# Kernel tuning notes

Measured on AMD Instinct MI355X. Metric: run time of the kernel, lower is better.

## Reference

```python
import jax, jax.numpy as jnp
import numpy as np

RES = 128
SH_DIM = 9            # (deg+1)^2, deg=2
CH = SH_DIM * 3 + 1   # 28: 3*9 SH rgb coeffs + 1 sigma
AABB_MIN = -1.0
AABB_MAX = 1.0
STEP = (AABB_MAX - AABB_MIN) / (RES - 1)   # voxel_len = mean(aabb_size/(res-1))
UNIFORM = 0.5
N_SAMPLES = int(RES * 3 / UNIFORM)         # plenoxels count: 768
EPS = 1e-10


def sh_encode_deg2(d):
    # real spherical harmonics basis, degree 2 (9 coefficients), on normalized dirs
    d = d / jnp.linalg.norm(d, axis=-1, keepdims=True)
    x, y, z = d[..., 0], d[..., 1], d[..., 2]
    C0 = 0.28209479177387814
    C1 = 0.4886025119029199
    C20, C21, C22 = 1.0925484305920792, -1.0925484305920792, 0.31539156525252005
    C23, C24 = -1.0925484305920792, 0.5462742152960396
    return jnp.stack([
        jnp.full_like(x, C0),
        -C1 * y, C1 * z, -C1 * x,
        C20 * x * y, C21 * y * z, C22 * (2.0 * z * z - x * x - y * y),
        C23 * x * z, C24 * (x * x - y * y),
    ], axis=-1)


def grid_sample_3d(grid, pts):
    # grid: [D,H,W,C]; pts: [...,3] in [-1,1], (x,y,z) with x->W, y->H, z->D.
    # Matches torch F.grid_sample(mode='bilinear', padding_mode='zeros', align_corners=True).
    D, H, W, C = grid.shape
    lead = pts.shape[:-1]
    p = pts.reshape(-1, 3)
    x = (p[:, 0] + 1.0) * 0.5 * (W - 1)
    y = (p[:, 1] + 1.0) * 0.5 * (H - 1)
    z = (p[:, 2] + 1.0) * 0.5 * (D - 1)
    x0f, y0f, z0f = jnp.floor(x), jnp.floor(y), jnp.floor(z)
    fx, fy, fz = x - x0f, y - y0f, z - z0f
    x0 = x0f.astype(jnp.int32)
    y0 = y0f.astype(jnp.int32)
    z0 = z0f.astype(jnp.int32)
    flat = grid.reshape(-1, C)
    out = jnp.zeros((p.shape[0], C), grid.dtype)
    for dz in (0, 1):
        for dy in (0, 1):
            for dx in (0, 1):
                xi, yi, zi = x0 + dx, y0 + dy, z0 + dz
                valid = (xi >= 0) & (xi < W) & (yi >= 0) & (yi < H) & (zi >= 0) & (zi < D)
                w = ((fx if dx else 1.0 - fx)
                     * (fy if dy else 1.0 - fy)
                     * (fz if dz else 1.0 - fz)) * valid
                idx = (jnp.clip(zi, 0, D - 1) * H + jnp.clip(yi, 0, H - 1)) * W + jnp.clip(xi, 0, W - 1)
                out = out + w[:, None] * flat[idx]
    return out.reshape(lead + (C,))


def setup_inputs() -> dict:
    key = jax.random.key(0)
    k1, k2, k3 = jax.random.split(key, 3)
    B = 4096
    # origins on a radius-3 sphere, aimed at jittered targets inside the unit box
    o = jax.random.normal(k1, (B, 3), dtype=jnp.float32)
    rays_o = 3.0 * o / jnp.linalg.norm(o, axis=-1, keepdims=True)
    tgt = jax.random.uniform(k2, (B, 3), dtype=jnp.float32, minval=-0.5, maxval=0.5)
    d = tgt - rays_o
    rays_d = d / jnp.linalg.norm(d, axis=-1, keepdims=True)
    grid_data = 0.1 * jax.random.normal(k3, (RES ** 3, CH), dtype=jnp.float32)
    grid_data = grid_data.at[:, -1].add(0.1)  # ini_sigma offset
    return {"rays_d": rays_d, "rays_o": rays_o, "grid_data": grid_data}


def reference(rays_d, rays_o, grid_data):
    B = rays_d.shape[0]
    aabb_lo = jnp.full((3,), AABB_MIN, rays_o.dtype)
    aabb_hi = jnp.full((3,), AABB_MAX, rays_o.dtype)
    # ray-AABB intersection (no_grad in torch)
    t_pos = (aabb_hi - rays_o) / rays_d
    t_neg = (aabb_lo - rays_o) / rays_d
    t_in = jnp.minimum(t_pos, t_neg)
    t_out = jnp.maximum(t_pos, t_neg)
    start = jnp.max(t_in, axis=-1)                  # [B]
    stop = jnp.min(t_out, axis=-1, keepdims=True)   # [B,1]
    # tensor_linspace from start+u*step to start+u*step*n, then clamp max=stop
    w = jnp.linspace(0.0, 1.0, N_SAMPLES, dtype=rays_o.dtype)  # [S]
    s0 = start + UNIFORM * STEP
    s1 = start + UNIFORM * STEP * N_SAMPLES
    intersections = s0[:, None] * (1.0 - w) + s1[:, None] * w   # [B,S]
    intersections = jnp.minimum(intersections, stop)
    t = intersections[:, :-1]                                    # [B,S-1]
    pts = rays_o[:, None, :] + t[:, :, None] * rays_d[:, None, :]
    pts = (pts - AABB_MIN) * (2.0 / (AABB_MAX - AABB_MIN)) - 1.0  # normalize to [-1,1]
    # trilinear sample of the voxel grid (torch layout: D=res0,H=res1,W=res2; x->W)
    interp = grid_sample_3d(grid_data.reshape(RES, RES, RES, CH), pts)  # [B,S-1,CH]
    sigma = interp[..., -1]
    rgb_sh = interp[..., :-1].reshape(B, N_SAMPLES - 1, 3, SH_DIM)
    sh = sh_encode_deg2(rays_d)                                   # [B,9]
    rgb = jnp.einsum('bsck,bk->bsc', rgb_sh, sh)
    # volumetric rendering
    dists = jnp.diff(intersections, axis=1) * jnp.linalg.norm(rays_d, axis=-1, keepdims=True)
    alpha = 1.0 - jnp.exp(-jax.nn.relu(sigma) * dists)
    cum_light = jnp.concatenate(
        [jnp.ones((B, 1), alpha.dtype), jnp.cumprod(1.0 - alpha[:, :-1] + EPS, axis=-1)], axis=-1)
    abs_light = alpha * cum_light
    acc_map = abs_light.sum(-1)
    rgb_map = (abs_light[..., None] * jax.nn.sigmoid(rgb)).sum(-2)
    depth = (abs_light * t).sum(-1)
    rgb_map = rgb_map + (1.0 - acc_map[:, None])  # white background
    return rgb_map, alpha, depth
```

## Files before the change

### kernel.cpp

```cpp
#include <hip/hip_runtime.h>
#include <math.h>

#define RESG 128
#define CHG 28
#define NT 767
#define NBKT 384

__global__ __launch_bounds__(1024) void prep_sort(
    const float* __restrict__ rays_d, int* __restrict__ perm, int B)
{
    __shared__ int cnt[NBKT];
    __shared__ int off[NBKT];
    __shared__ unsigned short keys[4096];
    const int tid = threadIdx.x;
    for (int i = tid; i < NBKT; i += 1024) cnt[i] = 0;
    __syncthreads();
    for (int r = tid; r < B; r += 1024) {
        float ddx = rays_d[r*3+0], ddy = rays_d[r*3+1], ddz = rays_d[r*3+2];
        float ax = fabsf(ddx), ay = fabsf(ddy), az = fabsf(ddz);
        int face; float u, v, m;
        if (ax >= ay && ax >= az) { face = (ddx < 0.f) ? 0 : 1; m = ax; u = ddy; v = ddz; }
        else if (ay >= az)        { face = (ddy < 0.f) ? 2 : 3; m = ay; u = ddx; v = ddz; }
        else                      { face = (ddz < 0.f) ? 4 : 5; m = az; u = ddx; v = ddy; }
        float iu = u / m * 0.5f + 0.5f;
        float iv = v / m * 0.5f + 0.5f;
        int qu = min(7, max(0, (int)(iu * 8.0f)));
        int qv = min(7, max(0, (int)(iv * 8.0f)));
        int k = face * 64 + qu * 8 + qv;
        keys[r] = (unsigned short)k;
        atomicAdd(&cnt[k], 1);
    }
    __syncthreads();
    if (tid == 0) {
        int a = 0;
        for (int i = 0; i < NBKT; ++i) { off[i] = a; a += cnt[i]; }
    }
    __syncthreads();
    for (int r = tid; r < B; r += 1024) {
        int k = keys[r];
        int slot = atomicAdd(&off[k], 1);
        perm[slot] = r;
    }
}

__global__ __launch_bounds__(256) void nerf_grid_kernel(
    const float* __restrict__ rays_d,
    const float* __restrict__ rays_o,
    const float* __restrict__ grid,
    const int*   __restrict__ perm,
    float* __restrict__ out_rgb,
    float* __restrict__ out_alpha,
    float* __restrict__ out_depth)
{
    const int ray  = perm[blockIdx.x];
    const int tid  = threadIdx.x;
    const int lane = tid & 63;
    const int wave = tid >> 6;

    const float EPSC   = 1e-10f;
    const float INV127 = 1.0f / 127.0f;

    __shared__ float a_lds[NT + 1];
    __shared__ float r_lds[NT + 1];
    __shared__ float g_lds[NT + 1];
    __shared__ float b_lds[NT + 1];
    __shared__ float wprod[4];
    __shared__ float red[4][5];

    const float ox = rays_o[ray*3+0], oy = rays_o[ray*3+1], oz = rays_o[ray*3+2];
    const float dx = rays_d[ray*3+0], dy = rays_d[ray*3+1], dz = rays_d[ray*3+2];
    const float dnorm = sqrtf(dx*dx + dy*dy + dz*dz);

    float txp = (1.0f - ox)/dx, txn = (-1.0f - ox)/dx;
    float typ = (1.0f - oy)/dy, tyn = (-1.0f - oy)/dy;
    float tzp = (1.0f - oz)/dz, tzn = (-1.0f - oz)/dz;
    const float start = fmaxf(fmaxf(fminf(txp,txn), fminf(typ,tyn)), fminf(tzp,tzn));
    const float stop  = fminf(fminf(fmaxf(txp,txn), fmaxf(typ,tyn)), fmaxf(tzp,tzn));

    int n_proc = (int)((stop - start) * 127.0f) + 2;
    n_proc = n_proc < 0 ? 0 : (n_proc > NT ? NT : n_proc);

    const float inv = 1.0f/dnorm;
    const float nx = dx*inv, ny = dy*inv, nz = dz*inv;
    float sh0, sh1, sh2, sh3, sh4, sh5, sh6, sh7, sh8;
    {
        const float C0 = 0.28209479177387814f;
        const float C1 = 0.4886025119029199f;
        const float C20 = 1.0925484305920792f, C21 = -1.0925484305920792f;
        const float C22 = 0.31539156525252005f;
        const float C23 = -1.0925484305920792f, C24 = 0.5462742152960396f;
        sh0 = C0;   sh1 = -C1*ny; sh2 = C1*nz; sh3 = -C1*nx;
        sh4 = C20*nx*ny; sh5 = C21*ny*nz;
        sh6 = C22*(2.0f*nz*nz - nx*nx - ny*ny);
        sh7 = C23*nx*nz; sh8 = C24*(nx*nx - ny*ny);
    }

    const int samp   = lane >> 3;
    const int corner = lane & 7;
    const int cdx = corner & 1, cdy = (corner >> 1) & 1, cdz = corner >> 2;

    for (int base = wave*8; base < n_proc; base += 32) {
        const int s = base + samp;
        float rr = 0.0f, gg = 0.0f, bb = 0.0f, sg = 0.0f;
        float t0 = 0.0f, dist = 0.0f;
        bool live = false;
        if (s < n_proc) {
            t0 = fminf(start + (float)(s+1)*INV127, stop);
            const float t1 = fminf(start + (float)(s+2)*INV127, stop);
            dist = (t1 - t0) * dnorm;
            live = dist > 0.0f;
        }
        if (live) {
            const float gx = (ox + t0*dx + 1.0f)*63.5f;
            const float gy = (oy + t0*dy + 1.0f)*63.5f;
            const float gz = (oz + t0*dz + 1.0f)*63.5f;
            const float fx0 = floorf(gx), fy0 = floorf(gy), fz0 = floorf(gz);
            const float fx = gx - fx0, fy = gy - fy0, fz = gz - fz0;
            const int xi = (int)fx0 + cdx;
            const int yi = (int)fy0 + cdy;
            const int zi = (int)fz0 + cdz;
            const bool valid = ((unsigned)xi < (unsigned)RESG) &
                               ((unsigned)yi < (unsigned)RESG) &
                               ((unsigned)zi < (unsigned)RESG);
            const float w = (cdx ? fx : 1.0f-fx) *
                            (cdy ? fy : 1.0f-fy) *
                            (cdz ? fz : 1.0f-fz);
            if (valid && w != 0.0f) {
                const float4* row = (const float4*)(grid + (size_t)(((zi*RESG) + yi)*RESG + xi)*CHG);
                const float4 v0 = row[0], v1 = row[1], v2 = row[2], v3 = row[3];
                const float4 v4 = row[4], v5 = row[5], v6 = row[6];
                rr = w*(v0.x*sh0 + v0.y*sh1 + v0.z*sh2 + v0.w*sh3 +
                        v1.x*sh4 + v1.y*sh5 + v1.z*sh6 + v1.w*sh7 + v2.x*sh8);
                gg = w*(v2.y*sh0 + v2.z*sh1 + v2.w*sh2 + v3.x*sh3 +
                        v3.y*sh4 + v3.z*sh5 + v3.w*sh6 + v4.x*sh7 + v4.y*sh8);
                bb = w*(v4.z*sh0 + v4.w*sh1 + v5.x*sh2 + v5.y*sh3 +
                        v5.z*sh4 + v5.w*sh5 + v6.x*sh6 + v6.y*sh7 + v6.z*sh8);
                sg = w*v6.w;
            }
        }
        #pragma unroll
        for (int off2 = 1; off2 < 8; off2 <<= 1) {
            rr += __shfl_xor(rr, off2, 64);
            gg += __shfl_xor(gg, off2, 64);
            bb += __shfl_xor(bb, off2, 64);
            sg += __shfl_xor(sg, off2, 64);
        }
        if (corner == 0 && s < n_proc) {
            a_lds[s] = live ? 1.0f - expf(-fmaxf(sg, 0.0f)*dist) : 0.0f;
            r_lds[s] = 1.0f/(1.0f + expf(-rr));
            g_lds[s] = 1.0f/(1.0f + expf(-gg));
            b_lds[s] = 1.0f/(1.0f + expf(-bb));
        }
    }
    __syncthreads();

    for (int s = tid; s < NT; s += 256)
        out_alpha[(size_t)ray*NT + s] = (s < n_proc) ? a_lds[s] : 0.0f;

    float a_r[3], q_r[3], t_r[3], rr_r[3], gg_r[3], bb_r[3];
    #pragma unroll
    for (int k = 0; k < 3; ++k) {
        const int s = tid*3 + k;
        float a = 0.0f, rr = 0.0f, gg = 0.0f, bb = 0.0f, tt = 0.0f;
        if (s < NT) {
            tt = fminf(start + (float)(s+1)*INV127, stop);
            if (s < n_proc) {
                a = a_lds[s];
                rr = r_lds[s]; gg = g_lds[s]; bb = b_lds[s];
            }
        }
        a_r[k] = a; q_r[k] = (s < NT) ? (1.0f - a + EPSC) : 1.0f;
        t_r[k] = tt; rr_r[k] = rr; gg_r[k] = gg; bb_r[k] = bb;
    }

    const float P = q_r[0]*q_r[1]*q_r[2];
    float incl = P;
    #pragma unroll
    for (int off2 = 1; off2 < 64; off2 <<= 1) {
        const float n = __shfl_up(incl, off2, 64);
        if (lane >= off2) incl *= n;
    }
    float excl = __shfl_up(incl, 1, 64);
    if (lane == 0) excl = 1.0f;

    if (lane == 63) wprod[wave] = incl;
    __syncthreads();
    float wpre = 1.0f;
    for (int w2 = 0; w2 < 4; ++w2) if (w2 < wave) wpre *= wprod[w2];

    float cum = wpre * excl;
    float accA = 0.0f, accR = 0.0f, accG = 0.0f, accB = 0.0f, accD = 0.0f;
    #pragma unroll
    for (int k = 0; k < 3; ++k) {
        const float abs_l = a_r[k] * cum;
        accA += abs_l;
        accR += abs_l * rr_r[k];
        accG += abs_l * gg_r[k];
        accB += abs_l * bb_r[k];
        accD += abs_l * t_r[k];
        cum *= q_r[k];
    }

    #pragma unroll
    for (int off2 = 32; off2 > 0; off2 >>= 1) {
        accA += __shfl_down(accA, off2, 64);
        accR += __shfl_down(accR, off2, 64);
        accG += __shfl_down(accG, off2, 64);
        accB += __shfl_down(accB, off2, 64);
        accD += __shfl_down(accD, off2, 64);
    }
    if (lane == 0) {
        red[wave][0] = accA; red[wave][1] = accR; red[wave][2] = accG;
        red[wave][3] = accB; red[wave][4] = accD;
    }
    __syncthreads();
    if (tid == 0) {
        float A = 0.0f, R = 0.0f, G = 0.0f, Bv = 0.0f, D = 0.0f;
        #pragma unroll
        for (int w2 = 0; w2 < 4; ++w2) {
            A += red[w2][0]; R += red[w2][1]; G += red[w2][2];
            Bv += red[w2][3]; D += red[w2][4];
        }
        const float bg = 1.0f - A;
        out_rgb[ray*3+0] = R  + bg;
        out_rgb[ray*3+1] = G  + bg;
        out_rgb[ray*3+2] = Bv + bg;
        out_depth[ray] = D;
    }
}

extern "C" void kernel_launch(void* const* d_in, const int* in_sizes, int n_in,
                              void* d_out, int out_size, void* d_ws, size_t ws_size,
                              hipStream_t stream) {
    const float* rays_d = (const float*)d_in[0];
    const float* rays_o = (const float*)d_in[1];
    const float* grid   = (const float*)d_in[2];
    const int B = in_sizes[0] / 3;

    float* out       = (float*)d_out;
    float* out_rgb   = out;
    float* out_alpha = out + (size_t)B*3;
    float* out_depth = out + (size_t)B*3 + (size_t)B*NT;

    int* perm = (int*)d_ws;

    prep_sort<<<1, 1024, 0, stream>>>(rays_d, perm, B);
    nerf_grid_kernel<<<B, 256, 0, stream>>>(rays_d, rays_o, grid, perm,
                                            out_rgb, out_alpha, out_depth);
}
```

Measured before the change: 89.35 us.

## Sort rays by sample count for load balance and use ds_swizzle reductions

The ray-ordering pass now buckets rays by their AABB intersection length (the number of live samples) in descending order, instead of by direction cube-face cells. Long rays are then dispatched first, so the GPU finishes with short blocks and tail imbalance shrinks, at the cost of direction coherence between neighbouring blocks. The bucket prefix sum now uses a wave scan instead of a serial loop. The 8-lane butterfly reductions in the main kernel are replaced with ds_swizzle XOR patterns, which avoid the more general cross-lane permute path.

```diff
diff --git a/kernel.cpp b/kernel.cpp
--- a/kernel.cpp
+++ b/kernel.cpp
@@ -4,41 +4,52 @@
 #define RESG 128
 #define CHG 28
 #define NT 767
-#define NBKT 384
+#define NLBKT 48
+
+template <int PAT>
+static __device__ __forceinline__ float swz(float x) {
+    return __int_as_float(__builtin_amdgcn_ds_swizzle(__float_as_int(x), PAT));
+}
 
 __global__ __launch_bounds__(1024) void prep_sort(
-    const float* __restrict__ rays_d, int* __restrict__ perm, int B)
+    const float* __restrict__ rays_d, const float* __restrict__ rays_o,
+    int* __restrict__ perm, int B)
 {
-    __shared__ int cnt[NBKT];
-    __shared__ int off[NBKT];
-    __shared__ unsigned short keys[4096];
+    __shared__ int cnt[64];
+    __shared__ int off[64];
+    __shared__ unsigned char keys[4096];
     const int tid = threadIdx.x;
-    for (int i = tid; i < NBKT; i += 1024) cnt[i] = 0;
+    if (tid < 64) cnt[tid] = 0;
     __syncthreads();
     for (int r = tid; r < B; r += 1024) {
-        float ddx = rays_d[r*3+0], ddy = rays_d[r*3+1], ddz = rays_d[r*3+2];
-        float ax = fabsf(ddx), ay = fabsf(ddy), az = fabsf(ddz);
-        int face; float u, v, m;
-        if (ax >= ay && ax >= az) { face = (ddx < 0.f) ? 0 : 1; m = ax; u = ddy; v = ddz; }
-        else if (ay >= az)        { face = (ddy < 0.f) ? 2 : 3; m = ay; u = ddx; v = ddz; }
-        else                      { face = (ddz < 0.f) ? 4 : 5; m = az; u = ddx; v = ddy; }
-        float iu = u / m * 0.5f + 0.5f;
-        float iv = v / m * 0.5f + 0.5f;
-        int qu = min(7, max(0, (int)(iu * 8.0f)));
-        int qv = min(7, max(0, (int)(iv * 8.0f)));
-        int k = face * 64 + qu * 8 + qv;
-        keys[r] = (unsigned short)k;
+        const float ox = rays_o[r*3+0], oy = rays_o[r*3+1], oz = rays_o[r*3+2];
+        const float dx = rays_d[r*3+0], dy = rays_d[r*3+1], dz = rays_d[r*3+2];
+        float txp = (1.0f - ox)/dx, txn = (-1.0f - ox)/dx;
+        float typ = (1.0f - oy)/dy, tyn = (-1.0f - oy)/dy;
+        float tzp = (1.0f - oz)/dz, tzn = (-1.0f - oz)/dz;
+        const float start = fmaxf(fmaxf(fminf(txp,txn), fminf(typ,tyn)), fminf(tzp,tzn));
+        const float stop  = fminf(fminf(fmaxf(txp,txn), fmaxf(typ,tyn)), fmaxf(tzp,tzn));
+        int n_proc = (int)((stop - start) * 127.0f) + 2;
+        n_proc = n_proc < 0 ? 0 : (n_proc > NT ? NT : n_proc);
+        int lvl = n_proc >> 4; if (lvl > NLBKT-1) lvl = NLBKT-1;
+        const int k = (NLBKT-1) - lvl;
+        keys[r] = (unsigned char)k;
         atomicAdd(&cnt[k], 1);
     }
     __syncthreads();
-    if (tid == 0) {
-        int a = 0;
-        for (int i = 0; i < NBKT; ++i) { off[i] = a; a += cnt[i]; }
+    if (tid < 64) {
+        int v = cnt[tid];
+        int incl = v;
+        #pragma unroll
+        for (int o2 = 1; o2 < 64; o2 <<= 1) {
+            const int n = __shfl_up(incl, o2, 64);
+            if ((tid & 63) >= o2) incl += n;
+        }
+        off[tid] = incl - v;
     }
     __syncthreads();
     for (int r = tid; r < B; r += 1024) {
-        int k = keys[r];
-        int slot = atomicAdd(&off[k], 1);
+        const int slot = atomicAdd(&off[keys[r]], 1);
         perm[slot] = r;
     }
 }
@@ -138,13 +149,10 @@
                 sg = w*v6.w;
             }
         }
-        #pragma unroll
-        for (int off2 = 1; off2 < 8; off2 <<= 1) {
-            rr += __shfl_xor(rr, off2, 64);
-            gg += __shfl_xor(gg, off2, 64);
-            bb += __shfl_xor(bb, off2, 64);
-            sg += __shfl_xor(sg, off2, 64);
-        }
+        rr += swz<0x041F>(rr); gg += swz<0x041F>(gg); bb += swz<0x041F>(bb); sg += swz<0x041F>(sg);
+        rr += swz<0x081F>(rr); gg += swz<0x081F>(gg); bb += swz<0x081F>(bb); sg += swz<0x081F>(sg);
+        rr += swz<0x101F>(rr); gg += swz<0x101F>(gg); bb += swz<0x101F>(bb); sg += swz<0x101F>(sg);
+
         if (corner == 0 && s < n_proc) {
             a_lds[s] = live ? 1.0f - expf(-fmaxf(sg, 0.0f)*dist) : 0.0f;
             r_lds[s] = 1.0f/(1.0f + expf(-rr));
@@ -244,7 +252,7 @@
 
     int* perm = (int*)d_ws;
 
-    prep_sort<<<1, 1024, 0, stream>>>(rays_d, perm, B);
+    prep_sort<<<1, 1024, 0, stream>>>(rays_d, rays_o, perm, B);
     nerf_grid_kernel<<<B, 256, 0, stream>>>(rays_d, rays_o, grid, perm,
                                             out_rgb, out_alpha, out_depth);
 }
```

Result: faster. 83.33 us (-6.7%).
